# Optimization experiments

Measured on AMD Instinct MI355X. Metric: run time of the kernel, lower is better.

Reference implementation:

```python
import jax, jax.numpy as jnp
import numpy as np

N = 100000      # nodes
E = 1600000     # edges (avg degree 16)
IN = 128        # in_channels
H = 64          # hidden
C = 2           # num_classes
G = 256         # graphs in batch


def _glorot(key, shape):
    lim = np.sqrt(6.0 / (shape[0] + shape[1])).astype(np.float32)
    return jax.random.uniform(key, shape, jnp.float32, -lim, lim)


def setup_inputs() -> dict:
    key = jax.random.key(0)
    ks = jax.random.split(key, 8)
    x = jax.random.normal(ks[0], (N, IN), jnp.float32)
    edge_index = jax.random.randint(ks[1], (2, E), 0, N)
    batch = jnp.sort(jax.random.randint(ks[2], (N,), 0, G))
    W1 = _glorot(ks[3], (IN, H)); b1 = jnp.zeros((H,), jnp.float32)
    W2 = _glorot(ks[4], (H, H));  b2 = jnp.zeros((H,), jnp.float32)
    Wc1 = _glorot(ks[5], (H, H // 2)); bc1 = jnp.zeros((H // 2,), jnp.float32)
    Wc2 = _glorot(ks[6], (H // 2, C)); bc2 = jnp.zeros((C,), jnp.float32)
    return dict(x=x, edge_index=edge_index, batch=batch,
                W1=W1, b1=b1, W2=W2, b2=b2,
                Wc1=Wc1, bc1=bc1, Wc2=Wc2, bc2=bc2)


def gcn_conv(x, W, b, src, dst, n):
    """PyG GCNConv: linear -> symmetric-normalized scatter-add with self-loops."""
    h = x @ W                                   # [N, out]
    # degree over dst including the added self-loop (edge_weight = 1)
    deg = jax.ops.segment_sum(jnp.ones((src.shape[0],), h.dtype), dst,
                              num_segments=n) + 1.0
    dinv = jax.lax.rsqrt(deg)                   # deg^{-1/2}
    norm = dinv[src] * dinv[dst]                # [E]
    msg = norm[:, None] * h[src]                # gather + normalize
    out = jax.ops.segment_sum(msg, dst, num_segments=n)
    out = out + (dinv * dinv)[:, None] * h      # self-loop contribution
    return out + b


def reference(x, edge_index, batch, W1, b1, W2, b2, Wc1, bc1, Wc2, bc2):
    src, dst = edge_index[0], edge_index[1]
    h = jax.nn.relu(gcn_conv(x, W1, b1, src, dst, N))
    h = jax.nn.relu(gcn_conv(h, W2, b2, src, dst, N))
    # global mean pool over graph ids
    s = jax.ops.segment_sum(h, batch, num_segments=G)
    cnt = jax.ops.segment_sum(jnp.ones((N,), h.dtype), batch, num_segments=G)
    g = s / jnp.maximum(cnt, 1.0)[:, None]      # [G, H]
    return jax.nn.relu(g @ Wc1 + bc1) @ Wc2 + bc2  # [G, C]
```

## Files before the change

### kernel.cpp

```cpp
#include <hip/hip_runtime.h>

#define N_NODES 100000
#define N_EDGES 1600000
#define IN_CH   128
#define HID     64
#define NG      256
#define CAP     64
#define NXCD    8
#define XRANGE  (N_NODES / NXCD)
#define NSLICE  32
#define PERSLICE (N_EDGES / NSLICE)
#define LINB    ((N_NODES + 63) / 64)

typedef __attribute__((ext_vector_type(8))) short bf16x8;
typedef __attribute__((ext_vector_type(4))) float f32x4;

__device__ __forceinline__ unsigned short f2bf(float f) {
    union { float f; unsigned u; } v; v.f = f;
    unsigned r = v.u + 0x7FFF + ((v.u >> 16) & 1);
    return (unsigned short)(r >> 16);
}
__device__ __forceinline__ float bfval(unsigned short h) {
    return __uint_as_float((unsigned)h << 16);
}
__device__ __forceinline__ unsigned int f2bf2(float lo, float hi) {
    return (unsigned int)f2bf(lo) | ((unsigned int)f2bf(hi) << 16);
}
__device__ __forceinline__ float bf_lo(unsigned int p) { return __uint_as_float(p << 16); }
__device__ __forceinline__ float bf_hi(unsigned int p) { return __uint_as_float(p & 0xFFFF0000u); }

__global__ void k_wcvt(const float* __restrict__ W1, const float* __restrict__ W2,
                       unsigned short* __restrict__ W1hi, unsigned short* __restrict__ W1lo,
                       unsigned short* __restrict__ W2hi, unsigned short* __restrict__ W2lo) {
    int t = blockIdx.x * blockDim.x + threadIdx.x;
    if (t < 64 * IN_CH) {
        int e = t & 7, lane = (t >> 3) & 63, q = t >> 9;
        int kk = q >> 2, cb = q & 3, kg = lane >> 4, r = lane & 15;
        float v = W1[(kk * 32 + kg * 8 + e) * 64 + cb * 16 + r];
        unsigned short hh = f2bf(v);
        W1hi[t] = hh;
        W1lo[t] = f2bf(v - bfval(hh));
    } else if (t < 64 * IN_CH + 64 * HID) {
        int t2 = t - 64 * IN_CH;
        int e = t2 & 7, lane = (t2 >> 3) & 63, q = t2 >> 9;
        int kk = q >> 2, cb = q & 3, kg = lane >> 4, r = lane & 15;
        float v = W2[(kk * 32 + kg * 8 + e) * 64 + cb * 16 + r];
        unsigned short hh = f2bf(v);
        W2hi[t2] = hh;
        W2lo[t2] = f2bf(v - bfval(hh));
    }
}

__global__ void __launch_bounds__(1024) k_cntA(const int* __restrict__ dst,
                                               int* __restrict__ cnt32) {
    __shared__ int c[XRANGE];
    const int r = blockIdx.x & (NXCD - 1);
    const int s = blockIdx.x >> 3;
    const int lo = r * XRANGE;
    for (int j = threadIdx.x; j < XRANGE; j += 1024) c[j] = 0;
    __syncthreads();
    const int4* d4 = reinterpret_cast<const int4*>(dst + s * PERSLICE);
    for (int q = threadIdx.x; q < PERSLICE / 4; q += 1024) {
        int4 v = d4[q];
        int t;
        t = v.x - lo; if ((unsigned)t < XRANGE) atomicAdd(&c[t], 1);
        t = v.y - lo; if ((unsigned)t < XRANGE) atomicAdd(&c[t], 1);
        t = v.z - lo; if ((unsigned)t < XRANGE) atomicAdd(&c[t], 1);
        t = v.w - lo; if ((unsigned)t < XRANGE) atomicAdd(&c[t], 1);
    }
    __syncthreads();
    int* outp = cnt32 + (long)s * N_NODES + lo;
    for (int j = threadIdx.x; j < XRANGE; j += 1024) outp[j] = c[j];
}

__global__ void k_prep(int* __restrict__ cnt32, int* __restrict__ deg,
                       float* __restrict__ dinv, int* __restrict__ col,
                       const int* __restrict__ batch, int* __restrict__ start) {
    int i = blockIdx.x * blockDim.x + threadIdx.x;
    if (i >= N_NODES) return;
    int run = 0;
#pragma unroll
    for (int s = 0; s < NSLICE; ++s) {
        long idx = (long)s * N_NODES + i;
        int v = cnt32[idx];
        cnt32[idx] = run;
        run += v;
    }
    deg[i] = run;
    dinv[i] = rsqrtf((float)run + 1.0f);
    int n = run < CAP ? run : CAP;
    int n16 = (n + 15) & ~15;
    int* crow = col + (long)i * CAP;
    int self32 = i * 32;
    for (int p = n; p < n16; ++p) crow[p] = self32;
    int b = batch[i];
    int prev = (i == 0) ? -1 : batch[i - 1];
    for (int g = prev + 1; g <= b; ++g) start[g] = i;
    if (i == N_NODES - 1)
        for (int g = b + 1; g <= NG; ++g) start[g] = N_NODES;
}

__global__ void __launch_bounds__(1024) k_place(const int* __restrict__ src,
                                                const int* __restrict__ dst,
                                                const int* __restrict__ off32,
                                                int* __restrict__ col) {
    __shared__ int c[XRANGE];
    const int r = blockIdx.x & (NXCD - 1);
    const int s = blockIdx.x >> 3;
    const int lo = r * XRANGE;
    for (int j = threadIdx.x; j < XRANGE; j += 1024) c[j] = 0;
    __syncthreads();
    const int4* d4 = reinterpret_cast<const int4*>(dst + s * PERSLICE);
    const int4* s4 = reinterpret_cast<const int4*>(src + s * PERSLICE);
    const int* obase = off32 + (long)s * N_NODES;
    for (int q = threadIdx.x; q < PERSLICE / 4; q += 1024) {
        int4 v = d4[q];
        int4 u = s4[q];
        int t, p;
        t = v.x - lo;
        if ((unsigned)t < XRANGE) {
            p = atomicAdd(&c[t], 1) + obase[v.x];
            if (p < CAP) col[(long)v.x * CAP + p] = u.x * 32;
        }
        t = v.y - lo;
        if ((unsigned)t < XRANGE) {
            p = atomicAdd(&c[t], 1) + obase[v.y];
            if (p < CAP) col[(long)v.y * CAP + p] = u.y * 32;
        }
        t = v.z - lo;
        if ((unsigned)t < XRANGE) {
            p = atomicAdd(&c[t], 1) + obase[v.z];
            if (p < CAP) col[(long)v.z * CAP + p] = u.z * 32;
        }
        t = v.w - lo;
        if ((unsigned)t < XRANGE) {
            p = atomicAdd(&c[t], 1) + obase[v.w];
            if (p < CAP) col[(long)v.w * CAP + p] = u.w * 32;
        }
    }
}

template <int K>
__global__ void __launch_bounds__(256) k_linear(const float* __restrict__ x,
                                                const unsigned short* __restrict__ Whi,
                                                const unsigned short* __restrict__ Wlo,
                                                const float* __restrict__ dinv,
                                                unsigned short* __restrict__ hs) {
    __shared__ f32x4 red[2][64][8];
    const int tid  = threadIdx.x;
    const int wv   = tid >> 6;
    const int pair = wv >> 1;
    const int h    = wv & 1;
    const int lane = tid & 63;
    const int row16 = lane & 15;
    const int kg    = lane >> 4;
    const int n0 = (blockIdx.x * 2 + pair) * 32;
    const bool valid = (n0 < N_NODES);

    f32x4 acc[2][4];
#pragma unroll
    for (int bt = 0; bt < 2; ++bt)
#pragma unroll
        for (int cb = 0; cb < 4; ++cb) acc[bt][cb] = (f32x4){0.f, 0.f, 0.f, 0.f};

    const int NKK = K / 32;
    const int kkBeg = h * (NKK / 2);
    const int kkEnd = kkBeg + NKK / 2;

#pragma unroll
    for (int kk = kkBeg; kk < kkEnd; ++kk) {
        bf16x8 xhi0, xlo0, xhi1, xlo1;
        {
            int rr = n0 + row16;
            rr = rr < N_NODES ? rr : N_NODES - 1;
            const float* ap = x + (long)rr * K + kk * 32 + kg * 8;
            float4 b0 = *reinterpret_cast<const float4*>(ap);
            float4 b1 = *reinterpret_cast<const float4*>(ap + 4);
#define CVT(dsthi, dstlo, i, val) { unsigned short h_ = f2bf(val); dsthi[i] = (short)h_; \
                                    dstlo[i] = (short)f2bf((val) - bfval(h_)); }
            CVT(xhi0, xlo0, 0, b0.x) CVT(xhi0, xlo0, 1, b0.y)
            CVT(xhi0, xlo0, 2, b0.z) CVT(xhi0, xlo0, 3, b0.w)
            CVT(xhi0, xlo0, 4, b1.x) CVT(xhi0, xlo0, 5, b1.y)
            CVT(xhi0, xlo0, 6, b1.z) CVT(xhi0, xlo0, 7, b1.w)
        }
        {
            int rr = n0 + 16 + row16;
            rr = rr < N_NODES ? rr : N_NODES - 1;
            const float* ap = x + (long)rr * K + kk * 32 + kg * 8;
            float4 b0 = *reinterpret_cast<const float4*>(ap);
            float4 b1 = *reinterpret_cast<const float4*>(ap + 4);
            CVT(xhi1, xlo1, 0, b0.x) CVT(xhi1, xlo1, 1, b0.y)
            CVT(xhi1, xlo1, 2, b0.z) CVT(xhi1, xlo1, 3, b0.w)
            CVT(xhi1, xlo1, 4, b1.x) CVT(xhi1, xlo1, 5, b1.y)
            CVT(xhi1, xlo1, 6, b1.z) CVT(xhi1, xlo1, 7, b1.w)
#undef CVT
        }
#pragma unroll
        for (int cb = 0; cb < 4; ++cb) {
            long foff = (long)((kk * 4 + cb) * 64 + lane) * 8;
            bf16x8 wh = *reinterpret_cast<const bf16x8*>(Whi + foff);
            bf16x8 wl = *reinterpret_cast<const bf16x8*>(Wlo + foff);
            acc[0][cb] = __builtin_amdgcn_mfma_f32_16x16x32_bf16(wh, xhi0, acc[0][cb], 0, 0, 0);
            acc[0][cb] = __builtin_amdgcn_mfma_f32_16x16x32_bf16(wh, xlo0, acc[0][cb], 0, 0, 0);
            acc[0][cb] = __builtin_amdgcn_mfma_f32_16x16x32_bf16(wl, xhi0, acc[0][cb], 0, 0, 0);
            acc[1][cb] = __builtin_amdgcn_mfma_f32_16x16x32_bf16(wh, xhi1, acc[1][cb], 0, 0, 0);
            acc[1][cb] = __builtin_amdgcn_mfma_f32_16x16x32_bf16(wh, xlo1, acc[1][cb], 0, 0, 0);
            acc[1][cb] = __builtin_amdgcn_mfma_f32_16x16x32_bf16(wl, xhi1, acc[1][cb], 0, 0, 0);
        }
    }

    if (h == 1) {
#pragma unroll
        for (int bt = 0; bt < 2; ++bt)
#pragma unroll
            for (int cb = 0; cb < 4; ++cb) red[pair][lane][bt * 4 + cb] = acc[bt][cb];
    }
    __syncthreads();
    if (h == 0 && valid) {
#pragma unroll
        for (int bt = 0; bt < 2; ++bt) {
            int n = n0 + bt * 16 + row16;
            float d = dinv[n];
#pragma unroll
            for (int cb = 0; cb < 4; ++cb) {
                f32x4 a = acc[bt][cb];
                f32x4 b = red[pair][lane][bt * 4 + cb];
                uint2 p;
                p.x = f2bf2((a[0] + b[0]) * d, (a[1] + b[1]) * d);
                p.y = f2bf2((a[2] + b[2]) * d, (a[3] + b[3]) * d);
                *reinterpret_cast<uint2*>(&hs[(long)n * 64 + cb * 16 + kg * 4]) = p;
            }
        }
    }
}

__global__ void k_gather(const int* __restrict__ deg, const int* __restrict__ col,
                         const unsigned int* __restrict__ hs2,
                         const float* __restrict__ dinv, const float* __restrict__ bias,
                         float* __restrict__ out) {
    int t = blockIdx.x * blockDim.x + threadIdx.x;
    int lane = t & 63;
    int half = lane >> 5;
    int c2 = lane & 31;
    int i = ((t >> 6) << 1) + half;
    if (i >= N_NODES) return;
    const int4* crow4 = reinterpret_cast<const int4*>(col + (long)i * CAP);
    int n = deg[i];
    n = n < CAP ? n : CAP;
    int n16 = (n + 15) & ~15;
    const unsigned int* hsc = hs2 + c2;
    unsigned int self = hsc[(long)i * 32];
    float selfL = bf_lo(self), selfH = bf_hi(self);
    float aL = selfL, aH = selfH;

    for (int e0 = 0; e0 < n16; e0 += 16) {
        int4 q0 = crow4[(e0 >> 2) + 0];
        int4 q1 = crow4[(e0 >> 2) + 1];
        int4 q2 = crow4[(e0 >> 2) + 2];
        int4 q3 = crow4[(e0 >> 2) + 3];
        unsigned int v[16];
        v[0]  = hsc[(long)q0.x]; v[1]  = hsc[(long)q0.y];
        v[2]  = hsc[(long)q0.z]; v[3]  = hsc[(long)q0.w];
        v[4]  = hsc[(long)q1.x]; v[5]  = hsc[(long)q1.y];
        v[6]  = hsc[(long)q1.z]; v[7]  = hsc[(long)q1.w];
        v[8]  = hsc[(long)q2.x]; v[9]  = hsc[(long)q2.y];
        v[10] = hsc[(long)q2.z]; v[11] = hsc[(long)q2.w];
        v[12] = hsc[(long)q3.x]; v[13] = hsc[(long)q3.y];
        v[14] = hsc[(long)q3.z]; v[15] = hsc[(long)q3.w];
#pragma unroll
        for (int j = 0; j < 16; ++j) {
            aL += bf_lo(v[j]);
            aH += bf_hi(v[j]);
        }
    }
    float fE = (float)(n16 - n);
    aL = fmaf(-fE, selfL, aL);
    aH = fmaf(-fE, selfH, aH);

    float di = dinv[i];
    float vL = fmaf(di, aL, bias[2 * c2]);
    float vH = fmaf(di, aH, bias[2 * c2 + 1]);
    float2 o;
    o.x = vL > 0.f ? vL : 0.f;
    o.y = vH > 0.f ? vH : 0.f;
    *reinterpret_cast<float2*>(&out[(long)i * 64 + 2 * c2]) = o;
}

__global__ void k_poolhead(const float* __restrict__ a, const int* __restrict__ start,
                           const float* __restrict__ Wc1, const float* __restrict__ bc1,
                           const float* __restrict__ Wc2, const float* __restrict__ bc2,
                           float* __restrict__ out) {
    __shared__ float partial[4][64];
    __shared__ float gvec[64];
    __shared__ float tvec[32];
    int g = blockIdx.x;
    int w = threadIdx.x >> 6;
    int j = threadIdx.x & 63;
    int s0 = start[g], s1 = start[g + 1];
    float acc = 0.f;
    for (int i = s0 + w; i < s1; i += 4)
        acc += a[(long)i * 64 + j];
    partial[w][j] = acc;
    __syncthreads();
    if (w == 0) {
        float c = (float)(s1 - s0);
        c = c > 1.f ? c : 1.f;
        gvec[j] = (partial[0][j] + partial[1][j] + partial[2][j] + partial[3][j]) / c;
    }
    __syncthreads();
    if (threadIdx.x < 32) {
        int jj = threadIdx.x;
        float acc2 = bc1[jj];
#pragma unroll 8
        for (int k = 0; k < 64; ++k) acc2 = fmaf(gvec[k], Wc1[k * 32 + jj], acc2);
        tvec[jj] = acc2 > 0.f ? acc2 : 0.f;
    }
    __syncthreads();
    if (threadIdx.x < 2) {
        int jj = threadIdx.x;
        float acc2 = bc2[jj];
#pragma unroll
        for (int k = 0; k < 32; ++k) acc2 = fmaf(tvec[k], Wc2[k * 2 + jj], acc2);
        out[g * 2 + jj] = acc2;
    }
}

extern "C" void kernel_launch(void* const* d_in, const int* in_sizes, int n_in,
                              void* d_out, int out_size, void* d_ws, size_t ws_size,
                              hipStream_t stream) {
    const float* x    = (const float*)d_in[0];
    const int*   ei   = (const int*)d_in[1];
    const int*   batch= (const int*)d_in[2];
    const float* W1   = (const float*)d_in[3];
    const float* b1   = (const float*)d_in[4];
    const float* W2   = (const float*)d_in[5];
    const float* b2   = (const float*)d_in[6];
    const float* Wc1  = (const float*)d_in[7];
    const float* bc1  = (const float*)d_in[8];
    const float* Wc2  = (const float*)d_in[9];
    const float* bc2  = (const float*)d_in[10];
    float* out = (float*)d_out;

    const int* src = ei;
    const int* dst = ei + N_EDGES;

    char* ws = (char*)d_ws;
    size_t off = 0;
    auto alloc = [&](size_t bytes) {
        void* p = ws + off;
        off += (bytes + 255) & ~(size_t)255;
        return p;
    };
    unsigned short* hs = (unsigned short*)alloc((size_t)N_NODES * HID * 2);
    float* agg     = (float*)alloc((size_t)N_NODES * HID * sizeof(float));
    int*   col     = (int*)  alloc((size_t)N_NODES * CAP * sizeof(int) + 256);
    int*   cnt32   = (int*)  alloc((size_t)NSLICE * N_NODES * sizeof(int));
    float* dinv    = (float*)alloc(N_NODES * sizeof(float));
    int*   deg     = (int*)  alloc(N_NODES * sizeof(int));
    int*   start   = (int*)  alloc((NG + 1) * sizeof(int));
    unsigned short* W1hi = (unsigned short*)alloc(64 * IN_CH * 2);
    unsigned short* W1lo = (unsigned short*)alloc(64 * IN_CH * 2);
    unsigned short* W2hi = (unsigned short*)alloc(64 * HID * 2);
    unsigned short* W2lo = (unsigned short*)alloc(64 * HID * 2);

    const int TB = 256;

    k_wcvt<<<(64 * (IN_CH + HID) + TB - 1) / TB, TB, 0, stream>>>(W1, W2, W1hi, W1lo, W2hi, W2lo);

    k_cntA<<<NXCD * NSLICE, 1024, 0, stream>>>(dst, cnt32);
    k_prep<<<(N_NODES + TB - 1) / TB, TB, 0, stream>>>(cnt32, deg, dinv, col, batch, start);
    k_place<<<NXCD * NSLICE, 1024, 0, stream>>>(src, dst, cnt32, col);

    const int gatherBlocks = ((N_NODES + 1) / 2 * 64 + TB - 1) / TB;

    k_linear<IN_CH><<<LINB, TB, 0, stream>>>(x, W1hi, W1lo, dinv, hs);
    k_gather<<<gatherBlocks, TB, 0, stream>>>(deg, col, (const unsigned int*)hs, dinv, b1, agg);

    k_linear<HID><<<LINB, TB, 0, stream>>>(agg, W2hi, W2lo, dinv, hs);
    k_gather<<<gatherBlocks, TB, 0, stream>>>(deg, col, (const unsigned int*)hs, dinv, b2, agg);

    k_poolhead<<<NG, 256, 0, stream>>>(agg, start, Wc1, bc1, Wc2, bc2, out);
}
```

Measured before the change: 194.6 us.

## Fuse layer-1 gather with layer-2 linear and record edge slots during counting

The first-layer aggregation is merged with the second-layer MFMA linear in one kernel. Each block gathers 64 nodes into shared memory, applies bias and ReLU, and multiplies by W2 there, so the fp32 agg round trip through global memory and one launch go away. Separately, the counting pass now saves each edge's local slot as a 16-bit value, so the placement kernel becomes a flat per-edge scatter without the second pass of LDS atomics. The cost is an extra pos array written and read, and the fused kernel's gather phase has only 256 threads per 64 nodes, which may reduce the memory parallelism available for the irregular gathers.

Measured after the change: 192.6 us. No clear change (-1.0%).

```diff
diff --git a/kernel.cpp b/kernel.cpp
--- a/kernel.cpp
+++ b/kernel.cpp
@@ -52,7 +52,8 @@
 }
 
 __global__ void __launch_bounds__(1024) k_cntA(const int* __restrict__ dst,
-                                               int* __restrict__ cnt32) {
+                                               int* __restrict__ cnt32,
+                                               unsigned short* __restrict__ pos) {
     __shared__ int c[XRANGE];
     const int r = blockIdx.x & (NXCD - 1);
     const int s = blockIdx.x >> 3;
@@ -60,13 +61,14 @@
     for (int j = threadIdx.x; j < XRANGE; j += 1024) c[j] = 0;
     __syncthreads();
     const int4* d4 = reinterpret_cast<const int4*>(dst + s * PERSLICE);
+    unsigned short* pp = pos + s * PERSLICE;
     for (int q = threadIdx.x; q < PERSLICE / 4; q += 1024) {
         int4 v = d4[q];
         int t;
-        t = v.x - lo; if ((unsigned)t < XRANGE) atomicAdd(&c[t], 1);
-        t = v.y - lo; if ((unsigned)t < XRANGE) atomicAdd(&c[t], 1);
-        t = v.z - lo; if ((unsigned)t < XRANGE) atomicAdd(&c[t], 1);
-        t = v.w - lo; if ((unsigned)t < XRANGE) atomicAdd(&c[t], 1);
+        t = v.x - lo; if ((unsigned)t < XRANGE) pp[q * 4 + 0] = (unsigned short)atomicAdd(&c[t], 1);
+        t = v.y - lo; if ((unsigned)t < XRANGE) pp[q * 4 + 1] = (unsigned short)atomicAdd(&c[t], 1);
+        t = v.z - lo; if ((unsigned)t < XRANGE) pp[q * 4 + 2] = (unsigned short)atomicAdd(&c[t], 1);
+        t = v.w - lo; if ((unsigned)t < XRANGE) pp[q * 4 + 3] = (unsigned short)atomicAdd(&c[t], 1);
     }
     __syncthreads();
     int* outp = cnt32 + (long)s * N_NODES + lo;
@@ -100,43 +102,15 @@
         for (int g = b + 1; g <= NG; ++g) start[g] = N_NODES;
 }
 
-__global__ void __launch_bounds__(1024) k_place(const int* __restrict__ src,
-                                                const int* __restrict__ dst,
-                                                const int* __restrict__ off32,
-                                                int* __restrict__ col) {
-    __shared__ int c[XRANGE];
-    const int r = blockIdx.x & (NXCD - 1);
-    const int s = blockIdx.x >> 3;
-    const int lo = r * XRANGE;
-    for (int j = threadIdx.x; j < XRANGE; j += 1024) c[j] = 0;
-    __syncthreads();
-    const int4* d4 = reinterpret_cast<const int4*>(dst + s * PERSLICE);
-    const int4* s4 = reinterpret_cast<const int4*>(src + s * PERSLICE);
-    const int* obase = off32 + (long)s * N_NODES;
-    for (int q = threadIdx.x; q < PERSLICE / 4; q += 1024) {
-        int4 v = d4[q];
-        int4 u = s4[q];
-        int t, p;
-        t = v.x - lo;
-        if ((unsigned)t < XRANGE) {
-            p = atomicAdd(&c[t], 1) + obase[v.x];
-            if (p < CAP) col[(long)v.x * CAP + p] = u.x * 32;
-        }
-        t = v.y - lo;
-        if ((unsigned)t < XRANGE) {
-            p = atomicAdd(&c[t], 1) + obase[v.y];
-            if (p < CAP) col[(long)v.y * CAP + p] = u.y * 32;
-        }
-        t = v.z - lo;
-        if ((unsigned)t < XRANGE) {
-            p = atomicAdd(&c[t], 1) + obase[v.z];
-            if (p < CAP) col[(long)v.z * CAP + p] = u.z * 32;
-        }
-        t = v.w - lo;
-        if ((unsigned)t < XRANGE) {
-            p = atomicAdd(&c[t], 1) + obase[v.w];
-            if (p < CAP) col[(long)v.w * CAP + p] = u.w * 32;
-        }
+__global__ void k_place(const int* __restrict__ src, const int* __restrict__ dst,
+                        const unsigned short* __restrict__ pos,
+                        const int* __restrict__ off32, int* __restrict__ col) {
+    const int stride = gridDim.x * blockDim.x;
+    for (int e = blockIdx.x * blockDim.x + threadIdx.x; e < N_EDGES; e += stride) {
+        int d = dst[e];
+        int s = e / PERSLICE;
+        int p = off32[(long)s * N_NODES + d] + (int)pos[e];
+        if (p < CAP) col[(long)d * CAP + p] = src[e] * 32;
     }
 }
 
@@ -193,7 +167,6 @@
             CVT(xhi1, xlo1, 2, b0.z) CVT(xhi1, xlo1, 3, b0.w)
             CVT(xhi1, xlo1, 4, b1.x) CVT(xhi1, xlo1, 5, b1.y)
             CVT(xhi1, xlo1, 6, b1.z) CVT(xhi1, xlo1, 7, b1.w)
-#undef CVT
         }
 #pragma unroll
         for (int cb = 0; cb < 4; ++cb) {
@@ -229,6 +202,141 @@
                 p.x = f2bf2((a[0] + b[0]) * d, (a[1] + b[1]) * d);
                 p.y = f2bf2((a[2] + b[2]) * d, (a[3] + b[3]) * d);
                 *reinterpret_cast<uint2*>(&hs[(long)n * 64 + cb * 16 + kg * 4]) = p;
+            }
+        }
+    }
+}
+
+__global__ void __launch_bounds__(256) k_gl(const int* __restrict__ deg,
+        const int* __restrict__ col, const unsigned int* __restrict__ hs2,
+        const float* __restrict__ dinv, const float* __restrict__ bias,
+        const unsigned short* __restrict__ Whi, const unsigned short* __restrict__ Wlo,
+        unsigned short* __restrict__ hsout) {
+    __shared__ float xg[64][68];
+    __shared__ f32x4 red[2][64][8];
+    const int tid  = threadIdx.x;
+    const int wv   = tid >> 6;
+    const int lane = tid & 63;
+    const int half = lane >> 5;
+    const int c2   = lane & 31;
+    const int n0 = blockIdx.x * 64;
+
+    for (int p8 = 0; p8 < 8; ++p8) {
+        int iw = p8 * 8 + wv * 2 + half;
+        int i = n0 + iw;
+        float oL = 0.f, oH = 0.f;
+        if (i < N_NODES) {
+            const int4* crow4 = reinterpret_cast<const int4*>(col + (long)i * CAP);
+            int n = deg[i];
+            n = n < CAP ? n : CAP;
+            int n16 = (n + 15) & ~15;
+            const unsigned int* hsc = hs2 + c2;
+            unsigned int self = hsc[(long)i * 32];
+            float selfL = bf_lo(self), selfH = bf_hi(self);
+            float aL = selfL, aH = selfH;
+            for (int e0 = 0; e0 < n16; e0 += 16) {
+                int4 q0 = crow4[(e0 >> 2) + 0];
+                int4 q1 = crow4[(e0 >> 2) + 1];
+                int4 q2 = crow4[(e0 >> 2) + 2];
+                int4 q3 = crow4[(e0 >> 2) + 3];
+                unsigned int v[16];
+                v[0]  = hsc[(long)q0.x]; v[1]  = hsc[(long)q0.y];
+                v[2]  = hsc[(long)q0.z]; v[3]  = hsc[(long)q0.w];
+                v[4]  = hsc[(long)q1.x]; v[5]  = hsc[(long)q1.y];
+                v[6]  = hsc[(long)q1.z]; v[7]  = hsc[(long)q1.w];
+                v[8]  = hsc[(long)q2.x]; v[9]  = hsc[(long)q2.y];
+                v[10] = hsc[(long)q2.z]; v[11] = hsc[(long)q2.w];
+                v[12] = hsc[(long)q3.x]; v[13] = hsc[(long)q3.y];
+                v[14] = hsc[(long)q3.z]; v[15] = hsc[(long)q3.w];
+#pragma unroll
+                for (int j = 0; j < 16; ++j) {
+                    aL += bf_lo(v[j]);
+                    aH += bf_hi(v[j]);
+                }
+            }
+            float fE = (float)(n16 - n);
+            aL = fmaf(-fE, selfL, aL);
+            aH = fmaf(-fE, selfH, aH);
+            float di = dinv[i];
+            float vL = fmaf(di, aL, bias[2 * c2]);
+            float vH = fmaf(di, aH, bias[2 * c2 + 1]);
+            oL = vL > 0.f ? vL : 0.f;
+            oH = vH > 0.f ? vH : 0.f;
+        }
+        *reinterpret_cast<float2*>(&xg[iw][2 * c2]) = (float2){oL, oH};
+    }
+    __syncthreads();
+
+    const int pair = wv >> 1;
+    const int h    = wv & 1;
+    const int row16 = lane & 15;
+    const int kg    = lane >> 4;
+    const int nb = pair * 32;
+    const int n0p = n0 + nb;
+    const bool valid = (n0p < N_NODES);
+
+    f32x4 acc[2][4];
+#pragma unroll
+    for (int bt = 0; bt < 2; ++bt)
+#pragma unroll
+        for (int cb = 0; cb < 4; ++cb) acc[bt][cb] = (f32x4){0.f, 0.f, 0.f, 0.f};
+
+    {
+        const int kk = h;
+        bf16x8 xhi0, xlo0, xhi1, xlo1;
+        {
+            const float* ap = &xg[nb + row16][kk * 32 + kg * 8];
+            float4 b0 = *reinterpret_cast<const float4*>(ap);
+            float4 b1 = *reinterpret_cast<const float4*>(ap + 4);
+            CVT(xhi0, xlo0, 0, b0.x) CVT(xhi0, xlo0, 1, b0.y)
+            CVT(xhi0, xlo0, 2, b0.z) CVT(xhi0, xlo0, 3, b0.w)
+            CVT(xhi0, xlo0, 4, b1.x) CVT(xhi0, xlo0, 5, b1.y)
+            CVT(xhi0, xlo0, 6, b1.z) CVT(xhi0, xlo0, 7, b1.w)
+        }
+        {
+            const float* ap = &xg[nb + 16 + row16][kk * 32 + kg * 8];
+            float4 b0 = *reinterpret_cast<const float4*>(ap);
+            float4 b1 = *reinterpret_cast<const float4*>(ap + 4);
+            CVT(xhi1, xlo1, 0, b0.x) CVT(xhi1, xlo1, 1, b0.y)
+            CVT(xhi1, xlo1, 2, b0.z) CVT(xhi1, xlo1, 3, b0.w)
+            CVT(xhi1, xlo1, 4, b1.x) CVT(xhi1, xlo1, 5, b1.y)
+            CVT(xhi1, xlo1, 6, b1.z) CVT(xhi1, xlo1, 7, b1.w)
+#undef CVT
+        }
+#pragma unroll
+        for (int cb = 0; cb < 4; ++cb) {
+            long foff = (long)((kk * 4 + cb) * 64 + lane) * 8;
+            bf16x8 wh = *reinterpret_cast<const bf16x8*>(Whi + foff);
+            bf16x8 wl = *reinterpret_cast<const bf16x8*>(Wlo + foff);
+            acc[0][cb] = __builtin_amdgcn_mfma_f32_16x16x32_bf16(wh, xhi0, acc[0][cb], 0, 0, 0);
+            acc[0][cb] = __builtin_amdgcn_mfma_f32_16x16x32_bf16(wh, xlo0, acc[0][cb], 0, 0, 0);
+            acc[0][cb] = __builtin_amdgcn_mfma_f32_16x16x32_bf16(wl, xhi0, acc[0][cb], 0, 0, 0);
+            acc[1][cb] = __builtin_amdgcn_mfma_f32_16x16x32_bf16(wh, xhi1, acc[1][cb], 0, 0, 0);
+            acc[1][cb] = __builtin_amdgcn_mfma_f32_16x16x32_bf16(wh, xlo1, acc[1][cb], 0, 0, 0);
+            acc[1][cb] = __builtin_amdgcn_mfma_f32_16x16x32_bf16(wl, xhi1, acc[1][cb], 0, 0, 0);
+        }
+    }
+
+    if (h == 1) {
+#pragma unroll
+        for (int bt = 0; bt < 2; ++bt)
+#pragma unroll
+            for (int cb = 0; cb < 4; ++cb) red[pair][lane][bt * 4 + cb] = acc[bt][cb];
+    }
+    __syncthreads();
+    if (h == 0 && valid) {
+#pragma unroll
+        for (int bt = 0; bt < 2; ++bt) {
+            int n = n0p + bt * 16 + row16;
+            float d = dinv[n];
+#pragma unroll
+            for (int cb = 0; cb < 4; ++cb) {
+                f32x4 a = acc[bt][cb];
+                f32x4 b = red[pair][lane][bt * 4 + cb];
+                uint2 p;
+                p.x = f2bf2((a[0] + b[0]) * d, (a[1] + b[1]) * d);
+                p.y = f2bf2((a[2] + b[2]) * d, (a[3] + b[3]) * d);
+                *reinterpret_cast<uint2*>(&hsout[(long)n * 64 + cb * 16 + kg * 4]) = p;
             }
         }
     }
@@ -352,9 +460,11 @@
         return p;
     };
     unsigned short* hs = (unsigned short*)alloc((size_t)N_NODES * HID * 2);
+    unsigned short* hs2b = (unsigned short*)alloc((size_t)N_NODES * HID * 2);
     float* agg     = (float*)alloc((size_t)N_NODES * HID * sizeof(float));
     int*   col     = (int*)  alloc((size_t)N_NODES * CAP * sizeof(int) + 256);
     int*   cnt32   = (int*)  alloc((size_t)NSLICE * N_NODES * sizeof(int));
+    unsigned short* pos = (unsigned short*)alloc((size_t)N_EDGES * 2);
     float* dinv    = (float*)alloc(N_NODES * sizeof(float));
     int*   deg     = (int*)  alloc(N_NODES * sizeof(int));
     int*   start   = (int*)  alloc((NG + 1) * sizeof(int));
@@ -367,17 +477,18 @@
 
     k_wcvt<<<(64 * (IN_CH + HID) + TB - 1) / TB, TB, 0, stream>>>(W1, W2, W1hi, W1lo, W2hi, W2lo);
 
-    k_cntA<<<NXCD * NSLICE, 1024, 0, stream>>>(dst, cnt32);
+    k_cntA<<<NXCD * NSLICE, 1024, 0, stream>>>(dst, cnt32, pos);
     k_prep<<<(N_NODES + TB - 1) / TB, TB, 0, stream>>>(cnt32, deg, dinv, col, batch, start);
-    k_place<<<NXCD * NSLICE, 1024, 0, stream>>>(src, dst, cnt32, col);
+    k_place<<<2048, TB, 0, stream>>>(src, dst, pos, cnt32, col);
 
     const int gatherBlocks = ((N_NODES + 1) / 2 * 64 + TB - 1) / TB;
 
     k_linear<IN_CH><<<LINB, TB, 0, stream>>>(x, W1hi, W1lo, dinv, hs);
-    k_gather<<<gatherBlocks, TB, 0, stream>>>(deg, col, (const unsigned int*)hs, dinv, b1, agg);
-
-    k_linear<HID><<<LINB, TB, 0, stream>>>(agg, W2hi, W2lo, dinv, hs);
-    k_gather<<<gatherBlocks, TB, 0, stream>>>(deg, col, (const unsigned int*)hs, dinv, b2, agg);
+
+    k_gl<<<LINB, TB, 0, stream>>>(deg, col, (const unsigned int*)hs, dinv, b1,
+                                  W2hi, W2lo, hs2b);
+
+    k_gather<<<gatherBlocks, TB, 0, stream>>>(deg, col, (const unsigned int*)hs2b, dinv, b2, agg);
 
     k_poolhead<<<NG, 256, 0, stream>>>(agg, start, Wc1, bc1, Wc2, bc2, out);
 }
```

## Record per-edge slot positions during counting to simplify CSR placement

Applied to the files above, without the earlier changes.

The counting kernel now stores each edge's local atomic slot index as a 16-bit value. The placement kernel becomes a flat grid-stride loop over edges that adds this stored slot to the slice prefix offset, with no shared-memory atomics and no redundant rescan of dst by all 8 XCD-range blocks. This removes the eightfold read of dst and src in placement, at the cost of writing and reading an extra 3.2 MB position array. The scatter stores into col stay uncoalesced.

Measured after the change: 191.0 us. No clear change (-1.8%).

```diff
diff --git a/kernel.cpp b/kernel.cpp
--- a/kernel.cpp
+++ b/kernel.cpp
@@ -52,7 +52,8 @@
 }
 
 __global__ void __launch_bounds__(1024) k_cntA(const int* __restrict__ dst,
-                                               int* __restrict__ cnt32) {
+                                               int* __restrict__ cnt32,
+                                               unsigned short* __restrict__ pos) {
     __shared__ int c[XRANGE];
     const int r = blockIdx.x & (NXCD - 1);
     const int s = blockIdx.x >> 3;
@@ -60,13 +61,14 @@
     for (int j = threadIdx.x; j < XRANGE; j += 1024) c[j] = 0;
     __syncthreads();
     const int4* d4 = reinterpret_cast<const int4*>(dst + s * PERSLICE);
+    unsigned short* pp = pos + s * PERSLICE;
     for (int q = threadIdx.x; q < PERSLICE / 4; q += 1024) {
         int4 v = d4[q];
         int t;
-        t = v.x - lo; if ((unsigned)t < XRANGE) atomicAdd(&c[t], 1);
-        t = v.y - lo; if ((unsigned)t < XRANGE) atomicAdd(&c[t], 1);
-        t = v.z - lo; if ((unsigned)t < XRANGE) atomicAdd(&c[t], 1);
-        t = v.w - lo; if ((unsigned)t < XRANGE) atomicAdd(&c[t], 1);
+        t = v.x - lo; if ((unsigned)t < XRANGE) pp[q * 4 + 0] = (unsigned short)atomicAdd(&c[t], 1);
+        t = v.y - lo; if ((unsigned)t < XRANGE) pp[q * 4 + 1] = (unsigned short)atomicAdd(&c[t], 1);
+        t = v.z - lo; if ((unsigned)t < XRANGE) pp[q * 4 + 2] = (unsigned short)atomicAdd(&c[t], 1);
+        t = v.w - lo; if ((unsigned)t < XRANGE) pp[q * 4 + 3] = (unsigned short)atomicAdd(&c[t], 1);
     }
     __syncthreads();
     int* outp = cnt32 + (long)s * N_NODES + lo;
@@ -100,43 +102,15 @@
         for (int g = b + 1; g <= NG; ++g) start[g] = N_NODES;
 }
 
-__global__ void __launch_bounds__(1024) k_place(const int* __restrict__ src,
-                                                const int* __restrict__ dst,
-                                                const int* __restrict__ off32,
-                                                int* __restrict__ col) {
-    __shared__ int c[XRANGE];
-    const int r = blockIdx.x & (NXCD - 1);
-    const int s = blockIdx.x >> 3;
-    const int lo = r * XRANGE;
-    for (int j = threadIdx.x; j < XRANGE; j += 1024) c[j] = 0;
-    __syncthreads();
-    const int4* d4 = reinterpret_cast<const int4*>(dst + s * PERSLICE);
-    const int4* s4 = reinterpret_cast<const int4*>(src + s * PERSLICE);
-    const int* obase = off32 + (long)s * N_NODES;
-    for (int q = threadIdx.x; q < PERSLICE / 4; q += 1024) {
-        int4 v = d4[q];
-        int4 u = s4[q];
-        int t, p;
-        t = v.x - lo;
-        if ((unsigned)t < XRANGE) {
-            p = atomicAdd(&c[t], 1) + obase[v.x];
-            if (p < CAP) col[(long)v.x * CAP + p] = u.x * 32;
-        }
-        t = v.y - lo;
-        if ((unsigned)t < XRANGE) {
-            p = atomicAdd(&c[t], 1) + obase[v.y];
-            if (p < CAP) col[(long)v.y * CAP + p] = u.y * 32;
-        }
-        t = v.z - lo;
-        if ((unsigned)t < XRANGE) {
-            p = atomicAdd(&c[t], 1) + obase[v.z];
-            if (p < CAP) col[(long)v.z * CAP + p] = u.z * 32;
-        }
-        t = v.w - lo;
-        if ((unsigned)t < XRANGE) {
-            p = atomicAdd(&c[t], 1) + obase[v.w];
-            if (p < CAP) col[(long)v.w * CAP + p] = u.w * 32;
-        }
+__global__ void k_place(const int* __restrict__ src, const int* __restrict__ dst,
+                        const unsigned short* __restrict__ pos,
+                        const int* __restrict__ off32, int* __restrict__ col) {
+    const int stride = gridDim.x * blockDim.x;
+    for (int e = blockIdx.x * blockDim.x + threadIdx.x; e < N_EDGES; e += stride) {
+        int d = dst[e];
+        int s = e / PERSLICE;
+        int p = off32[(long)s * N_NODES + d] + (int)pos[e];
+        if (p < CAP) col[(long)d * CAP + p] = src[e] * 32;
     }
 }
 
@@ -355,6 +329,7 @@
     float* agg     = (float*)alloc((size_t)N_NODES * HID * sizeof(float));
     int*   col     = (int*)  alloc((size_t)N_NODES * CAP * sizeof(int) + 256);
     int*   cnt32   = (int*)  alloc((size_t)NSLICE * N_NODES * sizeof(int));
+    unsigned short* pos = (unsigned short*)alloc((size_t)N_EDGES * 2);
     float* dinv    = (float*)alloc(N_NODES * sizeof(float));
     int*   deg     = (int*)  alloc(N_NODES * sizeof(int));
     int*   start   = (int*)  alloc((NG + 1) * sizeof(int));
@@ -367,9 +342,9 @@
 
     k_wcvt<<<(64 * (IN_CH + HID) + TB - 1) / TB, TB, 0, stream>>>(W1, W2, W1hi, W1lo, W2hi, W2lo);
 
-    k_cntA<<<NXCD * NSLICE, 1024, 0, stream>>>(dst, cnt32);
+    k_cntA<<<NXCD * NSLICE, 1024, 0, stream>>>(dst, cnt32, pos);
     k_prep<<<(N_NODES + TB - 1) / TB, TB, 0, stream>>>(cnt32, deg, dinv, col, batch, start);
-    k_place<<<NXCD * NSLICE, 1024, 0, stream>>>(src, dst, cnt32, col);
+    k_place<<<2048, TB, 0, stream>>>(src, dst, pos, cnt32, col);
 
     const int gatherBlocks = ((N_NODES + 1) / 2 * 64 + TB - 1) / TB;
 
```
